# Optimization experiments

Hardware: AMD Instinct MI355X
Metric: run time of the kernel (lower is better)

The kernel has to match this reference:

```python
import jax, jax.numpy as jnp
import numpy as np

B, DIM, H, W = 8, 64, 128, 128
HEADS = 8
HID = DIM * 2          # ffn_expansion_factor = 2
DCONV = DIM // 4       # partial-conv channels
EPS_LN = 1e-5
EPS_NRM = 1e-12

def _conv(x, w, groups=1):
    # stride-1 conv, SAME padding (matches padding=1 for k=3, padding=0 for k=1)
    return jax.lax.conv_general_dilated(
        x, w, (1, 1), 'SAME',
        dimension_numbers=('NCHW', 'OIHW', 'NCHW'),
        feature_group_count=groups)

def _ln_channel(x, w, b):
    # WithBias LayerNorm over channel dim (to_3d puts c last, normalize last dim)
    mu = x.mean(axis=1, keepdims=True)
    var = ((x - mu) ** 2).mean(axis=1, keepdims=True)
    return (x - mu) / jnp.sqrt(var + EPS_LN) * w[None, :, None, None] + b[None, :, None, None]

def setup_inputs() -> dict:
    key = jax.random.key(0)
    ks = jax.random.split(key, 8)
    s = 0.02
    return {
        'x': jax.random.normal(ks[0], (B, DIM, H, W), jnp.float32),
        'ln1_w': jnp.ones((DIM,), jnp.float32),
        'ln1_b': jnp.zeros((DIM,), jnp.float32),
        'qkv_w': jax.random.normal(ks[1], (3 * DIM, DIM, 1, 1), jnp.float32) * s,
        'qkv_dw_w': jax.random.normal(ks[2], (3 * DIM, 1, 3, 3), jnp.float32) * s,
        'temperature': jnp.ones((HEADS, 1, 1), jnp.float32),
        'attn_mix': jnp.ones((2,), jnp.float32),
        'proj_w': jax.random.normal(ks[3], (DIM, DIM, 1, 1), jnp.float32) * s,
        'ln2_w': jnp.ones((DIM,), jnp.float32),
        'ln2_b': jnp.zeros((DIM,), jnp.float32),
        'pconv_w': jax.random.normal(ks[4], (DCONV, DCONV, 3, 3), jnp.float32) * s,
        'pin_w': jax.random.normal(ks[5], (2 * HID, DIM, 1, 1), jnp.float32) * s,
        'dw_w': jax.random.normal(ks[6], (HID, 1, 3, 3), jnp.float32) * s,
        'pout_w': jax.random.normal(ks[7], (DIM, HID, 1, 1), jnp.float32) * s,
    }

def reference(x, ln1_w, ln1_b, qkv_w, qkv_dw_w, temperature, attn_mix,
              proj_w, ln2_w, ln2_b, pconv_w, pin_w, dw_w, pout_w):
    b, c, h, w = x.shape
    ch = c // HEADS
    # ---- TwinPeakAttention on norm1(x) ----
    y = _ln_channel(x, ln1_w, ln1_b)
    qkv = _conv(_conv(y, qkv_w), qkv_dw_w, groups=3 * c)
    q, k, v = jnp.split(qkv, 3, axis=1)
    rs = lambda t: t.reshape(b, HEADS, ch, h * w)          # b head c (h w)
    q, k, v = rs(q), rs(k), rs(v)
    q = q / jnp.maximum(jnp.linalg.norm(q, axis=-1, keepdims=True), EPS_NRM)
    k = k / jnp.maximum(jnp.linalg.norm(k, axis=-1, keepdims=True), EPS_NRM)
    scores = jnp.einsum('bhcn,bhdn->bhcd', q, k)           # [b, head, ch, ch]
    attn_sm = jax.nn.softmax(scores * temperature[None], axis=-1)
    attn_relu = jnp.maximum(scores, 0.0) ** 2
    wmix = jax.nn.softmax(attn_mix)
    attn = wmix[0] * attn_sm + wmix[1] * attn_relu
    out = jnp.einsum('bhcd,bhdn->bhcn', attn, v).reshape(b, c, h, w)
    x = x + _conv(out, proj_w)
    # ---- FDFN on norm2(x) ----
    y = _ln_channel(x, ln2_w, ln2_b)
    y = jnp.concatenate([_conv(y[:, :DCONV], pconv_w), y[:, DCONV:]], axis=1)
    y = _conv(y, pin_w)                                    # [b, 2*HID, h, w]
    a, g = jnp.split(y, 2, axis=1)
    a = _conv(a, dw_w, groups=HID)
    y = _conv(jax.nn.gelu(a, approximate=False) * g, pout_w)
    return x + y
```

## Files before the change

### kernel.cpp

```cpp
#include <hip/hip_runtime.h>
#include <math.h>

#define NPIX 16384
#define B_ 8

typedef __attribute__((ext_vector_type(4))) float f32x4;
typedef __attribute__((ext_vector_type(8))) short bf16x8;
typedef __attribute__((ext_vector_type(4))) unsigned int u32x4;

__device__ inline unsigned short f2bf(float f) {
  unsigned int u = __builtin_bit_cast(unsigned int, f);
  return (unsigned short)((u + 0x7fffu + ((u >> 16) & 1u)) >> 16);
}
__device__ inline float bf2f(unsigned short h) {
  unsigned int u = ((unsigned int)h) << 16;
  return __builtin_bit_cast(float, u);
}
__device__ inline unsigned int pack2(unsigned short a, unsigned short b) {
  return (unsigned int)a | ((unsigned int)b << 16);
}
__device__ inline f32x4 mfma16(bf16x8 a, bf16x8 b, f32x4 c) {
  return __builtin_amdgcn_mfma_f32_16x16x32_bf16(a, b, c, 0, 0, 0);
}
__device__ inline void unpack8(u32x4 u, float* f) {
#pragma unroll
  for (int i = 0; i < 4; ++i) {
    unsigned int w = u[i];
    f[2 * i]     = __builtin_bit_cast(float, w << 16);
    f[2 * i + 1] = __builtin_bit_cast(float, w & 0xffff0000u);
  }
}


__global__ __launch_bounds__(256) void k0_prep(
    const float* __restrict__ wq, const float* __restrict__ lw,
    const float* __restrict__ lb, const float* __restrict__ pin,
    const float* __restrict__ pout, unsigned short* __restrict__ wq2,
    float* __restrict__ s1, float* __restrict__ s2,
    unsigned short* __restrict__ pinb, unsigned short* __restrict__ pob) {
  int bid = blockIdx.x, t = threadIdx.x;
  if (bid == 0) {
    if (t < 192) {
      int co = t;
      float a = 0.f, bsum = 0.f;
      for (int ci = 0; ci < 64; ++ci) {
        float w = wq[co * 64 + ci];
        unsigned short hb = f2bf(w * lw[ci]);
        wq2[co * 64 + ci] = hb;
        a += bf2f(hb);
        bsum = fmaf(w, lb[ci], bsum);
      }
      s1[co] = a;
      s2[co] = bsum;
    }
  } else if (bid <= 64) {
    int i = (bid - 1) * 256 + t;
    pinb[i] = f2bf(pin[i]);
  } else {
    int i = (bid - 65) * 256 + t;
    pob[i] = f2bf(pout[i]);
  }
}

__global__ __launch_bounds__(256) void k1_qkv(
    const float* __restrict__ x, const unsigned short* __restrict__ wq2,
    const float* __restrict__ s1, const float* __restrict__ s2,
    unsigned short* __restrict__ qkv) {
  __shared__ __align__(16) unsigned char lx[64 * 128];
  __shared__ float sumL[4][64], sqL[4][64], muL[64], rsL[64];
  __shared__ __align__(16) unsigned short epi[4][16][72];
  int t = threadIdx.x, blk = blockIdx.x;
  int b = blk >> 8, hw0 = (blk & 255) * 64;
  const float* xb = x + (size_t)b * 64 * NPIX + hw0;
  int p = t & 63, g8 = t >> 6;
  float psum = 0.f, psq = 0.f;
#pragma unroll
  for (int r = 0; r < 2; ++r) {
    int ci0 = g8 * 8 + r * 32;
    float v[8];
#pragma unroll
    for (int j = 0; j < 8; ++j) {
      v[j] = xb[(size_t)(ci0 + j) * NPIX + p];
      psum += v[j];
      psq = fmaf(v[j], v[j], psq);
    }
    u32x4 pk;
#pragma unroll
    for (int j = 0; j < 4; ++j) pk[j] = pack2(f2bf(v[2 * j]), f2bf(v[2 * j + 1]));
    unsigned int addr = ((unsigned)(p * 128 + ci0 * 2)) ^ ((p & 7) << 4);
    *(u32x4*)&lx[addr] = pk;
  }
  sumL[g8][p] = psum;
  sqL[g8][p] = psq;
  __syncthreads();
  if (t < 64) {
    float s = sumL[0][t] + sumL[1][t] + sumL[2][t] + sumL[3][t];
    float q = sqL[0][t] + sqL[1][t] + sqL[2][t] + sqL[3][t];
    float mu = s * (1.f / 64.f);
    float var = q * (1.f / 64.f) - mu * mu;
    muL[t] = mu;
    rsL[t] = rsqrtf(fmaxf(var, 0.f) + 1e-5f);
  }
  __syncthreads();
  int lane = t & 63, wv = t >> 6, l16 = lane & 15, g = lane >> 4;
  int co0 = wv * 48;
  bf16x8 A[3][2];
#pragma unroll
  for (int ct = 0; ct < 3; ++ct) {
    int co = co0 + ct * 16 + l16;
#pragma unroll
    for (int kh = 0; kh < 2; ++kh)
      A[ct][kh] = *(const bf16x8*)(wq2 + (size_t)co * 64 + kh * 32 + g * 8);
  }
  f32x4 acc[3][4];
#pragma unroll
  for (int ct = 0; ct < 3; ++ct)
#pragma unroll
    for (int nt = 0; nt < 4; ++nt) acc[ct][nt] = (f32x4)0.f;
#pragma unroll
  for (int nt = 0; nt < 4; ++nt) {
    int pp = nt * 16 + l16;
#pragma unroll
    for (int kh = 0; kh < 2; ++kh) {
      unsigned int addr = ((unsigned)(pp * 128 + (kh * 32 + g * 8) * 2)) ^ ((pp & 7) << 4);
      bf16x8 Bf = *(const bf16x8*)&lx[addr];
#pragma unroll
      for (int ct = 0; ct < 3; ++ct) acc[ct][nt] = mfma16(A[ct][kh], Bf, acc[ct][nt]);
    }
  }
  int row1 = hw0 >> 7, wb1 = hw0 & 127;
  unsigned short* ob = qkv + ((size_t)(b * 128 + row1) * 192) * 128 + wb1;
#pragma unroll
  for (int ct = 0; ct < 3; ++ct) {
#pragma unroll
    for (int r = 0; r < 4; ++r) {
      int co = co0 + ct * 16 + g * 4 + r;
      float s1v = s1[co], s2v = s2[co];
#pragma unroll
      for (int nt = 0; nt < 4; ++nt) {
        int pl = nt * 16 + l16;
        float val = (acc[ct][nt][r] - muL[pl] * s1v) * rsL[pl] + s2v;
        epi[wv][g * 4 + r][pl] = f2bf(val);
      }
    }
#pragma unroll
    for (int i = 0; i < 2; ++i) {
      int chunk = i * 64 + lane, co_l = chunk >> 3, oct = chunk & 7;
      u32x4 v = *(const u32x4*)&epi[wv][co_l][oct * 8];
      *(u32x4*)(ob + (size_t)(co0 + ct * 16 + co_l) * 128 + oct * 8) = v;
    }
  }
}

__global__ __launch_bounds__(256) void k2_dw3x3(
    const unsigned short* __restrict__ in, const float* __restrict__ w9,
    unsigned short* __restrict__ out) {
  int blk0 = blockIdx.x;
  int blk = (blk0 & 7) * 1536 + (blk0 >> 3);
  int id = blk * 256 + threadIdx.x;
  int oct = id & 15;
  int cr = id >> 4;
  int ch = cr % 192;
  int br = cr / 192;
  int row = br & 127;
  int w0 = oct * 8;
  const float* wp = w9 + ch * 9;
  float wgt[9];
#pragma unroll
  for (int j = 0; j < 9; ++j) wgt[j] = wp[j];
  float rowv[3][10];
#pragma unroll
  for (int dy = 0; dy < 3; ++dy) {
#pragma unroll
    for (int i = 0; i < 10; ++i) rowv[dy][i] = 0.f;
    int hh = row + dy - 1;
    if ((unsigned)hh < 128u) {
      const unsigned short* rp = in + ((size_t)(br + dy - 1) * 192 + ch) * 128 + w0;
      u32x4 m = *(const u32x4*)rp;
      unpack8(m, &rowv[dy][1]);
      if (w0 > 0) rowv[dy][0] = bf2f(rp[-1]);
      if (w0 < 120) rowv[dy][9] = bf2f(rp[8]);
    }
  }
  u32x4 res;
#pragma unroll
  for (int i = 0; i < 8; i += 2) {
    float a0 = 0.f, a1 = 0.f;
#pragma unroll
    for (int dy = 0; dy < 3; ++dy)
#pragma unroll
      for (int dx = 0; dx < 3; ++dx) {
        a0 = fmaf(wgt[dy * 3 + dx], rowv[dy][i + dx], a0);
        a1 = fmaf(wgt[dy * 3 + dx], rowv[dy][i + 1 + dx], a1);
      }
    res[i >> 1] = pack2(f2bf(a0), f2bf(a1));
  }
  *(u32x4*)(out + ((size_t)br * 192 + ch) * 128 + w0) = res;
}

__global__ __launch_bounds__(256) void k3a_mfma(
    const unsigned short* __restrict__ qkvd, float* __restrict__ parts) {
  __shared__ float red[4][640];
  int blk = blockIdx.x;
  int b = blk >> 6, chunk = blk & 63;
  int t = threadIdx.x;
  int lane = t & 63, wv = t >> 6, l16 = lane & 15, g = lane >> 4;
  const unsigned short* bb = qkvd + (size_t)(b * 128) * 192 * 128;
  int n0 = chunk * 256 + wv * 64;
  f32x4 S[4], QQ[4], KK[4];
#pragma unroll
  for (int i = 0; i < 4; ++i) { S[i] = (f32x4)0.f; QQ[i] = (f32x4)0.f; KK[i] = (f32x4)0.f; }
#pragma unroll
  for (int ks = 0; ks < 2; ++ks) {
    int k0 = n0 + ks * 32 + g * 8;
    int r = k0 >> 7, w = k0 & 127;
    const unsigned short* rowb = bb + ((size_t)r * 192) * 128 + w;
    bf16x8 Q[4], K[4];
#pragma unroll
    for (int t4 = 0; t4 < 4; ++t4) {
      Q[t4] = *(const bf16x8*)(rowb + (size_t)(t4 * 16 + l16) * 128);
      K[t4] = *(const bf16x8*)(rowb + (size_t)(64 + t4 * 16 + l16) * 128);
    }
#pragma unroll
    for (int t4 = 0; t4 < 4; ++t4) {
      S[t4]  = mfma16(Q[t4], K[t4], S[t4]);
      QQ[t4] = mfma16(Q[t4], Q[t4], QQ[t4]);
      KK[t4] = mfma16(K[t4], K[t4], KK[t4]);
    }
  }
  int hi = l16 >> 3;
#pragma unroll
  for (int t4 = 0; t4 < 4; ++t4) {
#pragma unroll
    for (int r = 0; r < 4; ++r) {
      int m = g * 4 + r;
      if ((m >> 3) == hi) {
        int head = 2 * t4 + hi;
        red[wv][head * 80 + 16 + (m & 7) * 8 + (l16 & 7)] = S[t4][r];
      }
      if (m == l16) {
        int c = t4 * 16 + l16;
        red[wv][(c >> 3) * 80 + (c & 7)] = QQ[t4][r];
        red[wv][(c >> 3) * 80 + 8 + (c & 7)] = KK[t4][r];
      }
    }
  }
  __syncthreads();
  float* pb = parts + (size_t)blk * 640;
  for (int i = t; i < 640; i += 256)
    pb[i] = red[0][i] + red[1][i] + red[2][i] + red[3][i];
}

__global__ __launch_bounds__(256) void k3bc(
    const float* __restrict__ parts, const float* __restrict__ temp,
    const float* __restrict__ mix, const float* __restrict__ pw,
    unsigned short* __restrict__ M) {
  int b = blockIdx.x, t = threadIdx.x;
  __shared__ float s[8][80];
  __shared__ float att[8][64];
  for (int i = t; i < 640; i += 256) {
    const float* pbase = parts + (size_t)b * 64 * 640 + i;
    float v = 0.f;
    for (int c = 0; c < 64; ++c) v += pbase[c * 640];
    s[i / 80][i % 80] = v;
  }
  __syncthreads();
  float m0 = fmaxf(mix[0], mix[1]);
  float e0 = expf(mix[0] - m0), e1 = expf(mix[1] - m0);
  float w0 = e0 / (e0 + e1), w1 = e1 / (e0 + e1);
  for (int i = t; i < 512; i += 256) {
    int head = i >> 6, e = i & 63, c = e >> 3, d = e & 7;
    float tt = temp[head];
    float rq = 1.f / fmaxf(sqrtf(s[head][c]), 1e-12f);
    float sc[8];
    float mx = -1e30f;
#pragma unroll
    for (int d2 = 0; d2 < 8; ++d2) {
      float rk = 1.f / fmaxf(sqrtf(s[head][8 + d2]), 1e-12f);
      sc[d2] = s[head][16 + c * 8 + d2] * rq * rk;
      mx = fmaxf(mx, sc[d2] * tt);
    }
    float sum = 0.f;
#pragma unroll
    for (int d2 = 0; d2 < 8; ++d2) sum += expf(sc[d2] * tt - mx);
    float sm = expf(sc[d] * tt - mx) / sum;
    float r = fmaxf(sc[d], 0.f);
    r = r * r;
    att[head][e] = w0 * sm + w1 * r;
  }
  __syncthreads();
  for (int i = t; i < 4096; i += 256) {
    int co = i >> 6, ci = i & 63, head = ci >> 3, d = ci & 7;
    float a = 0.f;
#pragma unroll
    for (int cc = 0; cc < 8; ++cc)
      a = fmaf(pw[co * 64 + head * 8 + cc], att[head][cc * 8 + d], a);
    M[(size_t)b * 4096 + i] = f2bf(a);
  }
}

__global__ __launch_bounds__(256) void k4_av(
    const unsigned short* __restrict__ qkvd, const unsigned short* __restrict__ Mb,
    const float* __restrict__ x, const float* __restrict__ lw,
    const float* __restrict__ lb, unsigned short* __restrict__ x1,
    unsigned short* __restrict__ y2) {
  __shared__ __align__(16) unsigned char lv[64 * 128];
  __shared__ float sumL[4][64], sqL[4][64], muL[64], rsL[64];
  __shared__ __align__(16) unsigned short epi[4][16][72];
  int t = threadIdx.x, blk = blockIdx.x;
  int b = blk >> 8, hw0 = (blk & 255) * 64;
  int row4 = hw0 >> 7, wb4 = hw0 & 127;
  const unsigned short* vb = qkvd + ((size_t)(b * 128 + row4) * 192 + 128) * 128 + wb4;
  int p = t & 63, g8 = t >> 6;
#pragma unroll
  for (int r = 0; r < 2; ++r) {
    int ci0 = g8 * 8 + r * 32;
    unsigned short hh[8];
#pragma unroll
    for (int j = 0; j < 8; ++j) hh[j] = vb[(size_t)(ci0 + j) * 128 + p];
    u32x4 pk;
#pragma unroll
    for (int j = 0; j < 4; ++j) pk[j] = pack2(hh[2 * j], hh[2 * j + 1]);
    unsigned int addr = ((unsigned)(p * 128 + ci0 * 2)) ^ ((p & 7) << 4);
    *(u32x4*)&lv[addr] = pk;
  }
  __syncthreads();
  int lane = t & 63, wv = t >> 6, l16 = lane & 15, g = lane >> 4;
  bf16x8 A[2];
#pragma unroll
  for (int kh = 0; kh < 2; ++kh)
    A[kh] = *(const bf16x8*)(Mb + (size_t)b * 4096 + (size_t)(wv * 16 + l16) * 64 + kh * 32 + g * 8);
  f32x4 acc[4];
#pragma unroll
  for (int nt = 0; nt < 4; ++nt) acc[nt] = (f32x4)0.f;
#pragma unroll
  for (int nt = 0; nt < 4; ++nt) {
    int pp = nt * 16 + l16;
#pragma unroll
    for (int kh = 0; kh < 2; ++kh) {
      unsigned int addr = ((unsigned)(pp * 128 + (kh * 32 + g * 8) * 2)) ^ ((pp & 7) << 4);
      bf16x8 Bf = *(const bf16x8*)&lv[addr];
      acc[nt] = mfma16(A[kh], Bf, acc[nt]);
    }
  }
  const float* xb = x + (size_t)b * 64 * NPIX + hw0;
  unsigned short* x1b = x1 + (size_t)b * 64 * NPIX + hw0;
  float vals[4][4];
#pragma unroll
  for (int nt = 0; nt < 4; ++nt) {
    float ps = 0.f, pq = 0.f;
#pragma unroll
    for (int r = 0; r < 4; ++r) {
      int co = wv * 16 + g * 4 + r;
      size_t idx = (size_t)co * NPIX + nt * 16 + l16;
      float a = acc[nt][r] + xb[idx];
      vals[nt][r] = a;
      epi[wv][g * 4 + r][nt * 16 + l16] = f2bf(a);
      ps += a;
      pq = fmaf(a, a, pq);
    }
    ps += __shfl_xor(ps, 16); ps += __shfl_xor(ps, 32);
    pq += __shfl_xor(pq, 16); pq += __shfl_xor(pq, 32);
    if (g == 0) { sumL[wv][nt * 16 + l16] = ps; sqL[wv][nt * 16 + l16] = pq; }
  }
#pragma unroll
  for (int i = 0; i < 2; ++i) {
    int chunk = i * 64 + lane, co_l = chunk >> 3, oct = chunk & 7;
    u32x4 v = *(const u32x4*)&epi[wv][co_l][oct * 8];
    *(u32x4*)(x1b + (size_t)(wv * 16 + co_l) * NPIX + oct * 8) = v;
  }
  __syncthreads();
  if (t < 64) {
    float s = sumL[0][t] + sumL[1][t] + sumL[2][t] + sumL[3][t];
    float q = sqL[0][t] + sqL[1][t] + sqL[2][t] + sqL[3][t];
    float mu = s * (1.f / 64.f);
    float var = q * (1.f / 64.f) - mu * mu;
    muL[t] = mu;
    rsL[t] = rsqrtf(fmaxf(var, 0.f) + 1e-5f);
  }
  __syncthreads();
  unsigned short* y2b = y2 + (size_t)b * 64 * NPIX + hw0;
#pragma unroll
  for (int nt = 0; nt < 4; ++nt)
#pragma unroll
    for (int r = 0; r < 4; ++r) {
      int co = wv * 16 + g * 4 + r;
      int pl = nt * 16 + l16;
      float yv = (vals[nt][r] - muL[pl]) * rsL[pl] * lw[co] + lb[co];
      epi[wv][g * 4 + r][pl] = f2bf(yv);
    }
#pragma unroll
  for (int i = 0; i < 2; ++i) {
    int chunk = i * 64 + lane, co_l = chunk >> 3, oct = chunk & 7;
    u32x4 v = *(const u32x4*)&epi[wv][co_l][oct * 8];
    *(u32x4*)(y2b + (size_t)(wv * 16 + co_l) * NPIX + oct * 8) = v;
  }
}

__global__ __launch_bounds__(256) void k5_pconv(
    const unsigned short* __restrict__ y2, const float* __restrict__ pcw,
    unsigned short* __restrict__ pc) {
  __shared__ unsigned short ly[16 * 120];
  int t = threadIdx.x, blk = blockIdx.x;
  int b = blk >> 8, tile = blk & 255;
  int ty = tile >> 4, tx = tile & 15;
  int h0 = ty * 8, w0 = tx * 8;
  const unsigned short* yb = y2 + (size_t)b * 64 * NPIX;
  for (int i = t; i < 1600; i += 256) {
    int ci = i / 100, r = i - ci * 100;
    int hy = r / 10, hx = r - hy * 10;
    int gh = h0 - 1 + hy, gw = w0 - 1 + hx;
    unsigned short v = 0;
    if ((unsigned)gh < 128u && (unsigned)gw < 128u) v = yb[(size_t)ci * NPIX + gh * 128 + gw];
    ly[ci * 120 + hy * 12 + hx] = v;
  }
  __syncthreads();
  int lp = t & 63;
  int py = lp >> 3, px = lp & 7;
  int cq = __builtin_amdgcn_readfirstlane(t >> 6);
  int co0 = cq * 4;
  float a0 = 0.f, a1 = 0.f, a2 = 0.f, a3 = 0.f;
  for (int ci = 0; ci < 16; ++ci) {
    float nb[9];
#pragma unroll
    for (int ky = 0; ky < 3; ++ky)
#pragma unroll
      for (int kx = 0; kx < 3; ++kx)
        nb[ky * 3 + kx] = bf2f(ly[ci * 120 + (py + ky) * 12 + px + kx]);
    const float* wp = pcw + (co0 * 16 + ci) * 9;
#pragma unroll
    for (int k = 0; k < 9; ++k) {
      a0 = fmaf(wp[k],       nb[k], a0);
      a1 = fmaf(wp[144 + k], nb[k], a1);
      a2 = fmaf(wp[288 + k], nb[k], a2);
      a3 = fmaf(wp[432 + k], nb[k], a3);
    }
  }
  size_t obase = (size_t)b * 16 * NPIX + (h0 + py) * 128 + w0 + px;
  pc[obase + (size_t)(co0 + 0) * NPIX] = f2bf(a0);
  pc[obase + (size_t)(co0 + 1) * NPIX] = f2bf(a1);
  pc[obase + (size_t)(co0 + 2) * NPIX] = f2bf(a2);
  pc[obase + (size_t)(co0 + 3) * NPIX] = f2bf(a3);
}

__global__ __launch_bounds__(256) void k6_pin(
    const unsigned short* __restrict__ pc, const unsigned short* __restrict__ y2,
    const unsigned short* __restrict__ pinb, unsigned short* __restrict__ ag) {
  __shared__ __align__(16) unsigned char bt[64 * 128];
  __shared__ __align__(16) unsigned short epi[4][16][72];
  int t = threadIdx.x, blk = blockIdx.x;
  int b = blk >> 8, hw0 = (blk & 255) * 64;
  int px = t & 63, cb = t >> 6;
  {
    const unsigned short* base = (cb == 0) ? (pc + (size_t)b * 16 * NPIX)
                                           : (y2 + (size_t)b * 64 * NPIX);
#pragma unroll
    for (int j = 0; j < 16; j += 2) {
      int ch = cb * 16 + j;
      unsigned short v0 = base[(size_t)ch * NPIX + hw0 + px];
      unsigned short v1 = base[(size_t)(ch + 1) * NPIX + hw0 + px];
      unsigned int addr = ((unsigned)(px * 128 + ch * 2)) ^ ((px & 7) << 4);
      *(unsigned int*)&bt[addr] = pack2(v0, v1);
    }
  }
  __syncthreads();
  int lane = t & 63, wv = t >> 6, l16 = lane & 15, g = lane >> 4;
  bf16x8 A[4][2];
#pragma unroll
  for (int ct = 0; ct < 4; ++ct) {
    int co = wv * 64 + ct * 16 + l16;
#pragma unroll
    for (int kh = 0; kh < 2; ++kh)
      A[ct][kh] = *(const bf16x8*)(pinb + (size_t)co * 64 + kh * 32 + g * 8);
  }
  f32x4 acc[4][4];
#pragma unroll
  for (int ct = 0; ct < 4; ++ct)
#pragma unroll
    for (int nt = 0; nt < 4; ++nt) acc[ct][nt] = (f32x4)0.f;
#pragma unroll
  for (int nt = 0; nt < 4; ++nt) {
    int pp = nt * 16 + l16;
#pragma unroll
    for (int kh = 0; kh < 2; ++kh) {
      unsigned int addr = ((unsigned)(pp * 128 + (kh * 32 + g * 8) * 2)) ^ ((pp & 7) << 4);
      bf16x8 Bf = *(const bf16x8*)&bt[addr];
#pragma unroll
      for (int ct = 0; ct < 4; ++ct) acc[ct][nt] = mfma16(A[ct][kh], Bf, acc[ct][nt]);
    }
  }
  int row6 = hw0 >> 7, wb6 = hw0 & 127;
  unsigned short* ab = ag + ((size_t)(b * 128 + row6) * 256) * 128 + wb6;
#pragma unroll
  for (int ct = 0; ct < 4; ++ct) {
#pragma unroll
    for (int nt = 0; nt < 4; ++nt)
#pragma unroll
      for (int r = 0; r < 4; ++r)
        epi[wv][g * 4 + r][nt * 16 + l16] = f2bf(acc[ct][nt][r]);
#pragma unroll
    for (int i = 0; i < 2; ++i) {
      int chunk = i * 64 + lane, co_l = chunk >> 3, oct = chunk & 7;
      u32x4 v = *(const u32x4*)&epi[wv][co_l][oct * 8];
      int co = wv * 64 + ct * 16 + co_l;
      *(u32x4*)(ab + (size_t)co * 128 + oct * 8) = v;
    }
  }
}

__global__ __launch_bounds__(256) void k7_fdfn(
    const unsigned short* __restrict__ ag, const float* __restrict__ dww,
    const unsigned short* __restrict__ pob, const unsigned short* __restrict__ x1,
    float* __restrict__ out) {
  __shared__ __align__(16) unsigned char bt[64 * 256];
  __shared__ float dwl[1152];
  int t = threadIdx.x;
  int blk0 = blockIdx.x;
  int blk = (blk0 & 7) * 256 + (blk0 >> 3);
  int b = blk >> 8, rr = blk & 255;
  int row = rr >> 1, w0t = (rr & 1) * 64;
  for (int i = t; i < 1152; i += 256) dwl[i] = dww[i];
  __syncthreads();
#pragma unroll 1
  for (int it = 0; it < 2; ++it) {
    int idx = it * 256 + t;
    int chp = idx >> 3, oct = idx & 7;
    int ch0 = chp * 2;
    int w0 = w0t + oct * 8;
    float rowa[2][3][10];
    float gt[2][8];
#pragma unroll
    for (int cc = 0; cc < 2; ++cc) {
      int ch = ch0 + cc;
#pragma unroll
      for (int dy = 0; dy < 3; ++dy) {
#pragma unroll
        for (int i2 = 0; i2 < 10; ++i2) rowa[cc][dy][i2] = 0.f;
        int hh = row + dy - 1;
        if ((unsigned)hh < 128u) {
          const unsigned short* rp = ag + ((size_t)(b * 128 + hh) * 256 + ch) * 128 + w0;
          unpack8(*(const u32x4*)rp, &rowa[cc][dy][1]);
          if (w0 > 0) rowa[cc][dy][0] = bf2f(rp[-1]);
          if (w0 < 120) rowa[cc][dy][9] = bf2f(rp[8]);
        }
      }
      unpack8(*(const u32x4*)(ag + ((size_t)(b * 128 + row) * 256 + 128 + ch) * 128 + w0), gt[cc]);
    }
    float wgt[2][9];
#pragma unroll
    for (int cc = 0; cc < 2; ++cc)
#pragma unroll
      for (int j = 0; j < 9; ++j) wgt[cc][j] = dwl[(ch0 + cc) * 9 + j];
#pragma unroll
    for (int i2 = 0; i2 < 8; ++i2) {
      unsigned short h2[2];
#pragma unroll
      for (int cc = 0; cc < 2; ++cc) {
        float a = 0.f;
#pragma unroll
        for (int dy = 0; dy < 3; ++dy)
#pragma unroll
          for (int dx = 0; dx < 3; ++dx)
            a = fmaf(wgt[cc][dy * 3 + dx], rowa[cc][dy][i2 + dx], a);
        float gl = 0.5f * a * (1.f + erff(a * 0.70710678118654752f)) * gt[cc][i2];
        h2[cc] = f2bf(gl);
      }
      int pxl = oct * 8 + i2;
      unsigned int f = (unsigned)(((pxl & 7) ^ (pxl >> 3)) << 4);
      unsigned int addr = (unsigned)(pxl * 256) + (((unsigned)(ch0 * 2)) ^ f);
      *(unsigned int*)&bt[addr] = pack2(h2[0], h2[1]);
    }
  }
  __syncthreads();
  int lane = t & 63, wv = t >> 6, l16 = lane & 15, g = lane >> 4;
  bf16x8 A[4];
#pragma unroll
  for (int kh = 0; kh < 4; ++kh)
    A[kh] = *(const bf16x8*)(pob + (size_t)(wv * 16 + l16) * 128 + kh * 32 + g * 8);
  f32x4 acc[4];
#pragma unroll
  for (int nt = 0; nt < 4; ++nt) acc[nt] = (f32x4)0.f;
#pragma unroll
  for (int nt = 0; nt < 4; ++nt) {
    int pp = nt * 16 + l16;
    unsigned int f = (unsigned)(((pp & 7) ^ (pp >> 3)) << 4);
#pragma unroll
    for (int kh = 0; kh < 4; ++kh) {
      unsigned int addr = (unsigned)(pp * 256) + (((unsigned)((kh * 32 + g * 8) * 2)) ^ f);
      bf16x8 Bf = *(const bf16x8*)&bt[addr];
      acc[nt] = mfma16(A[kh], Bf, acc[nt]);
    }
  }
  __syncthreads();
  float* ebuf = (float*)&bt[wv * 4096];
#pragma unroll
  for (int nt = 0; nt < 4; ++nt)
#pragma unroll
    for (int r = 0; r < 4; ++r)
      ebuf[(g * 4 + r) * 64 + nt * 16 + l16] = acc[nt][r];
  const unsigned short* x1b = x1 + (size_t)b * 64 * NPIX + row * 128 + w0t;
  float* ob = out + (size_t)b * 64 * NPIX + row * 128 + w0t;
#pragma unroll
  for (int i = 0; i < 4; ++i) {
    int chunk = i * 64 + lane;
    int co_l = chunk >> 4, q4 = (chunk & 15) * 4;
    f32x4 v = *(const f32x4*)&ebuf[co_l * 64 + q4];
    int co = wv * 16 + co_l;
    uint2 xv = *(const uint2*)(x1b + (size_t)co * NPIX + q4);
    f32x4 o;
    o[0] = v[0] + bf2f((unsigned short)(xv.x & 0xffffu));
    o[1] = v[1] + bf2f((unsigned short)(xv.x >> 16));
    o[2] = v[2] + bf2f((unsigned short)(xv.y & 0xffffu));
    o[3] = v[3] + bf2f((unsigned short)(xv.y >> 16));
    *(f32x4*)(ob + (size_t)co * NPIX + q4) = o;
  }
}

extern "C" void kernel_launch(void* const* d_in, const int* in_sizes, int n_in,
                              void* d_out, int out_size, void* d_ws, size_t ws_size,
                              hipStream_t stream) {
  const float* x       = (const float*)d_in[0];
  const float* ln1_w   = (const float*)d_in[1];
  const float* ln1_b   = (const float*)d_in[2];
  const float* qkv_w   = (const float*)d_in[3];
  const float* qkv_dww = (const float*)d_in[4];
  const float* temp    = (const float*)d_in[5];
  const float* mix     = (const float*)d_in[6];
  const float* proj_w  = (const float*)d_in[7];
  const float* ln2_w   = (const float*)d_in[8];
  const float* ln2_b   = (const float*)d_in[9];
  const float* pconv_w = (const float*)d_in[10];
  const float* pin_w   = (const float*)d_in[11];
  const float* dw_w    = (const float*)d_in[12];
  const float* pout_w  = (const float*)d_in[13];
  float* out = (float*)d_out;

  if (ws_size < (size_t)117515776) return;
  char* w8 = (char*)d_ws;
  unsigned short* qkv  = (unsigned short*)(w8 + 0);
  unsigned short* qkvd = (unsigned short*)(w8 + 50331648);
  unsigned short* x1   = (unsigned short*)(w8 + 100663296);
  unsigned short* wq2  = (unsigned short*)(w8 + 117440512);
  float*          s1   = (float*)(w8 + 117465088);
  float*          s2   = (float*)(w8 + 117465856);
  unsigned short* pinb = (unsigned short*)(w8 + 117466624);
  unsigned short* pob  = (unsigned short*)(w8 + 117499392);
  float*          parts= (float*)(w8 + 0);
  unsigned short* M    = (unsigned short*)(w8 + 2097152);
  unsigned short* y2   = (unsigned short*)(w8 + 4194304);
  unsigned short* pc   = (unsigned short*)(w8 + 20971520);
  unsigned short* ag   = (unsigned short*)(w8 + 33554432);

  k0_prep<<<97, 256, 0, stream>>>(qkv_w, ln1_w, ln1_b, pin_w, pout_w, wq2, s1, s2, pinb, pob);
  k1_qkv<<<2048, 256, 0, stream>>>(x, wq2, s1, s2, qkv);
  k2_dw3x3<<<12288, 256, 0, stream>>>(qkv, qkv_dww, qkvd);
  k3a_mfma<<<512, 256, 0, stream>>>(qkvd, parts);
  k3bc<<<8, 256, 0, stream>>>(parts, temp, mix, proj_w, M);
  k4_av<<<2048, 256, 0, stream>>>(qkvd, M, x, ln2_w, ln2_b, x1, y2);
  k5_pconv<<<2048, 256, 0, stream>>>(y2, pconv_w, pc);
  k6_pin<<<2048, 256, 0, stream>>>(pc, y2, pinb, ag);
  k7_fdfn<<<2048, 256, 0, stream>>>(ag, dw_w, pob, x1, out);
}
```

Before: 173.1 us.

## Split fused depthwise-GELU and output projection into two kernels

Separates the depthwise 3x3 conv plus GELU gating from the pout MFMA projection, writing an intermediate bf16 tensor to workspace. The first kernel uses one 8-pixel chunk per thread across 8192 blocks to raise parallelism and cut register pressure. The second kernel only loads the precomputed activations into LDS before the MFMA. This adds a full intermediate write and read through global memory.

```diff
diff --git a/kernel.cpp b/kernel.cpp
--- a/kernel.cpp
+++ b/kernel.cpp
@@ -508,67 +508,80 @@
   }
 }
 
-__global__ __launch_bounds__(256) void k7_fdfn(
+__global__ __launch_bounds__(256) void k7a_dwgelu(
     const unsigned short* __restrict__ ag, const float* __restrict__ dww,
-    const unsigned short* __restrict__ pob, const unsigned short* __restrict__ x1,
-    float* __restrict__ out) {
+    unsigned short* __restrict__ h) {
+  int blk0 = blockIdx.x;
+  int blk = (blk0 & 7) * 1024 + (blk0 >> 3);
+  int id = blk * 256 + threadIdx.x;
+  int oct = id & 15;
+  int cr = id >> 4;
+  int ch = cr & 127;
+  int br = cr >> 7;
+  int row = br & 127;
+  int w0 = oct * 8;
+  const float* wp = dww + ch * 9;
+  float wgt[9];
+#pragma unroll
+  for (int j = 0; j < 9; ++j) wgt[j] = wp[j];
+  float rowv[3][10];
+#pragma unroll
+  for (int dy = 0; dy < 3; ++dy) {
+#pragma unroll
+    for (int i = 0; i < 10; ++i) rowv[dy][i] = 0.f;
+    int hh = row + dy - 1;
+    if ((unsigned)hh < 128u) {
+      const unsigned short* rp = ag + ((size_t)(br + dy - 1) * 256 + ch) * 128 + w0;
+      unpack8(*(const u32x4*)rp, &rowv[dy][1]);
+      if (w0 > 0) rowv[dy][0] = bf2f(rp[-1]);
+      if (w0 < 120) rowv[dy][9] = bf2f(rp[8]);
+    }
+  }
+  float gt[8];
+  unpack8(*(const u32x4*)(ag + ((size_t)br * 256 + 128 + ch) * 128 + w0), gt);
+  u32x4 res;
+#pragma unroll
+  for (int i = 0; i < 8; i += 2) {
+    float a0 = 0.f, a1 = 0.f;
+#pragma unroll
+    for (int dy = 0; dy < 3; ++dy)
+#pragma unroll
+      for (int dx = 0; dx < 3; ++dx) {
+        a0 = fmaf(wgt[dy * 3 + dx], rowv[dy][i + dx], a0);
+        a1 = fmaf(wgt[dy * 3 + dx], rowv[dy][i + 1 + dx], a1);
+      }
+    float g0 = 0.5f * a0 * (1.f + erff(a0 * 0.70710678118654752f)) * gt[i];
+    float g1 = 0.5f * a1 * (1.f + erff(a1 * 0.70710678118654752f)) * gt[i + 1];
+    res[i >> 1] = pack2(f2bf(g0), f2bf(g1));
+  }
+  *(u32x4*)(h + ((size_t)br * 128 + ch) * 128 + w0) = res;
+}
+
+__global__ __launch_bounds__(256) void k7b_pout(
+    const unsigned short* __restrict__ h, const unsigned short* __restrict__ pob,
+    const unsigned short* __restrict__ x1, float* __restrict__ out) {
   __shared__ __align__(16) unsigned char bt[64 * 256];
-  __shared__ float dwl[1152];
   int t = threadIdx.x;
   int blk0 = blockIdx.x;
   int blk = (blk0 & 7) * 256 + (blk0 >> 3);
   int b = blk >> 8, rr = blk & 255;
   int row = rr >> 1, w0t = (rr & 1) * 64;
-  for (int i = t; i < 1152; i += 256) dwl[i] = dww[i];
-  __syncthreads();
-#pragma unroll 1
-  for (int it = 0; it < 2; ++it) {
-    int idx = it * 256 + t;
+  const unsigned short* hb = h + ((size_t)(b * 128 + row) * 128) * 128 + w0t;
+#pragma unroll
+  for (int p = 0; p < 2; ++p) {
+    int idx = p * 256 + t;
     int chp = idx >> 3, oct = idx & 7;
     int ch0 = chp * 2;
-    int w0 = w0t + oct * 8;
-    float rowa[2][3][10];
-    float gt[2][8];
-#pragma unroll
-    for (int cc = 0; cc < 2; ++cc) {
-      int ch = ch0 + cc;
-#pragma unroll
-      for (int dy = 0; dy < 3; ++dy) {
-#pragma unroll
-        for (int i2 = 0; i2 < 10; ++i2) rowa[cc][dy][i2] = 0.f;
-        int hh = row + dy - 1;
-        if ((unsigned)hh < 128u) {
-          const unsigned short* rp = ag + ((size_t)(b * 128 + hh) * 256 + ch) * 128 + w0;
-          unpack8(*(const u32x4*)rp, &rowa[cc][dy][1]);
-          if (w0 > 0) rowa[cc][dy][0] = bf2f(rp[-1]);
-          if (w0 < 120) rowa[cc][dy][9] = bf2f(rp[8]);
-        }
-      }
-      unpack8(*(const u32x4*)(ag + ((size_t)(b * 128 + row) * 256 + 128 + ch) * 128 + w0), gt[cc]);
-    }
-    float wgt[2][9];
-#pragma unroll
-    for (int cc = 0; cc < 2; ++cc)
-#pragma unroll
-      for (int j = 0; j < 9; ++j) wgt[cc][j] = dwl[(ch0 + cc) * 9 + j];
+    u32x4 av = *(const u32x4*)(hb + (size_t)ch0 * 128 + oct * 8);
+    u32x4 bv = *(const u32x4*)(hb + (size_t)(ch0 + 1) * 128 + oct * 8);
 #pragma unroll
     for (int i2 = 0; i2 < 8; ++i2) {
-      unsigned short h2[2];
-#pragma unroll
-      for (int cc = 0; cc < 2; ++cc) {
-        float a = 0.f;
-#pragma unroll
-        for (int dy = 0; dy < 3; ++dy)
-#pragma unroll
-          for (int dx = 0; dx < 3; ++dx)
-            a = fmaf(wgt[cc][dy * 3 + dx], rowa[cc][dy][i2 + dx], a);
-        float gl = 0.5f * a * (1.f + erff(a * 0.70710678118654752f)) * gt[cc][i2];
-        h2[cc] = f2bf(gl);
-      }
+      unsigned short a16 = (unsigned short)((av[i2 >> 1] >> ((i2 & 1) * 16)) & 0xffffu);
+      unsigned short b16 = (unsigned short)((bv[i2 >> 1] >> ((i2 & 1) * 16)) & 0xffffu);
       int pxl = oct * 8 + i2;
       unsigned int f = (unsigned)(((pxl & 7) ^ (pxl >> 3)) << 4);
       unsigned int addr = (unsigned)(pxl * 256) + (((unsigned)(ch0 * 2)) ^ f);
-      *(unsigned int*)&bt[addr] = pack2(h2[0], h2[1]);
+      *(unsigned int*)&bt[addr] = pack2(a16, b16);
     }
   }
   __syncthreads();
@@ -650,6 +663,7 @@
   unsigned short* y2   = (unsigned short*)(w8 + 4194304);
   unsigned short* pc   = (unsigned short*)(w8 + 20971520);
   unsigned short* ag   = (unsigned short*)(w8 + 33554432);
+  unsigned short* h    = (unsigned short*)(w8 + 0);
 
   k0_prep<<<97, 256, 0, stream>>>(qkv_w, ln1_w, ln1_b, pin_w, pout_w, wq2, s1, s2, pinb, pob);
   k1_qkv<<<2048, 256, 0, stream>>>(x, wq2, s1, s2, qkv);
@@ -659,5 +673,6 @@
   k4_av<<<2048, 256, 0, stream>>>(qkvd, M, x, ln2_w, ln2_b, x1, y2);
   k5_pconv<<<2048, 256, 0, stream>>>(y2, pconv_w, pc);
   k6_pin<<<2048, 256, 0, stream>>>(pc, y2, pinb, ag);
-  k7_fdfn<<<2048, 256, 0, stream>>>(ag, dw_w, pob, x1, out);
-}
+  k7a_dwgelu<<<8192, 256, 0, stream>>>(ag, dw_w, h);
+  k7b_pout<<<2048, 256, 0, stream>>>(h, pob, x1, out);
+}
```

After: 177.7 us. 1.03x slower.
